# Performance work log

Hardware: AMD Instinct MI355X
Metric: run time of the kernel (lower is better)

## Reference

```python
import jax, jax.numpy as jnp
import numpy as np

D, L, H, DK, DV = 768, 512, 12, 64, 64
EPS = 1e-6

def setup_inputs() -> dict:
    key = jax.random.key(0)
    ks = jax.random.split(key, 14)
    def xn(k, shape):
        # xavier_normal: std = sqrt(2/(fan_in+fan_out))
        std = (2.0 / (shape[0] + shape[1])) ** 0.5
        return jax.random.normal(k, shape, dtype=jnp.float32) * std
    B = 8
    return {
        "Q": jax.random.normal(ks[0], (B, L, D), dtype=jnp.float32),
        "K": jax.random.normal(ks[1], (B, L, D), dtype=jnp.float32),
        "V": jax.random.normal(ks[2], (B, L, D), dtype=jnp.float32),
        "W_q": xn(ks[3], (D, H * DK)),
        "W_k": xn(ks[4], (D, H * DK)),
        "W_v": xn(ks[5], (D, H * DV)),
        "W_pos": xn(ks[6], (L, L)),
        "W_neg": xn(ks[7], (L, L)),
        "W_o": xn(ks[8], (H * DV, D)),
        "W_o2": xn(ks[9], (H * DV, D)),
        "w1": xn(ks[10], (D, D)),
        "b1": jnp.zeros((D,), dtype=jnp.float32),
        "w2": xn(ks[11], (D, D)),
        "b2": jnp.zeros((D,), dtype=jnp.float32),
    }

def reference(Q, K, V, W_q, W_k, W_v, W_pos, W_neg, W_o, W_o2, w1, b1, w2, b2):
    B, Lq, _ = Q.shape
    q = (Q @ W_q).reshape(B, Lq, H, DK)  # [B,L,H,dk]
    k = (K @ W_k).reshape(B, Lq, H, DK)
    v = (V @ W_v).reshape(B, Lq, H, DV)
    temp = DK ** 0.5 + EPS
    QK = jnp.einsum('bqhd,bkhd->bhqk', q, k) / temp  # [B,H,L,L]
    # einsum 'bqk,kk->bqk' == multiply by diagonal of W_pos/W_neg along key axis
    dpos = jnp.diagonal(W_pos)  # [L]
    dneg = jnp.diagonal(W_neg)
    sp = jax.nn.softmax(QK * dpos, axis=-1)
    sn = -jax.nn.softmax(-(QK * dneg), axis=-1)
    Vp = jnp.einsum('bhqk,bkhd->bqhd', sp, v).reshape(B, Lq, H * DV)
    Vn = jnp.einsum('bhqk,bkhd->bqhd', sn, v).reshape(B, Lq, H * DV)
    out_pos = Vp @ W_o
    out_neg = Vn @ W_o2
    def ffn(X):
        return jax.nn.relu(X @ w1 + b1) @ w2 + b2
    X_pos = Q + out_pos
    X_neg = Q + out_neg
    return (ffn(X_pos) + X_pos, ffn(X_neg) + X_neg)
```

## Files before the change

kernel.cpp:

```cpp
#include <hip/hip_runtime.h>
#include <hip/hip_bf16.h>
#include <math.h>

typedef __bf16 bf16_t;
typedef __bf16 bf16x4 __attribute__((ext_vector_type(4)));
typedef __bf16 bf16x8 __attribute__((ext_vector_type(8)));
typedef float f32x4 __attribute__((ext_vector_type(4)));

#define MFMA16(a, b, c) __builtin_amdgcn_mfma_f32_16x16x32_bf16((a), (b), (c), 0, 0, 0)
#define EXP2F(x) __builtin_amdgcn_exp2f(x)

__device__ __forceinline__ void gll16(const void* g, void* lds) {
    __builtin_amdgcn_global_load_lds((const __attribute__((address_space(1))) void*)g,
                                     (__attribute__((address_space(3))) void*)lds, 16, 0, 0);
}

struct PrepPtrs {
    const float* csrc[3];
    bf16_t* cdst[3];
    const float* wsrc[7];
    bf16_t* wdst[7];
};

__global__ __launch_bounds__(256) void prep_kernel(PrepPtrs p) {
    const int bx = blockIdx.x, tid = threadIdx.x;
    if (bx < 4608) {
        const int t = bx / 1536, i = (bx - t * 1536) * 256 + tid;
        const float4 u = ((const float4*)p.csrc[t])[i * 2];
        const float4 v = ((const float4*)p.csrc[t])[i * 2 + 1];
        bf16x8 o;
        o[0] = (bf16_t)u.x; o[1] = (bf16_t)u.y; o[2] = (bf16_t)u.z; o[3] = (bf16_t)u.w;
        o[4] = (bf16_t)v.x; o[5] = (bf16_t)v.y; o[6] = (bf16_t)v.z; o[7] = (bf16_t)v.w;
        ((bf16x8*)p.cdst[t])[i] = o;
    } else {
        __shared__ float t[32][33];
        const int q = bx - 4608, wz = q / 576, rem = q - wz * 576;
        const int bxx = rem % 24, byy = rem / 24;
        const float* src = p.wsrc[wz];
        bf16_t* dst = p.wdst[wz];
        const int tx = tid & 31, ty = tid >> 5;
        const int x = bxx * 32 + tx;
        const int y0 = byy * 32;
#pragma unroll
        for (int j = 0; j < 4; ++j)
            t[ty + j * 8][tx] = src[(size_t)(y0 + ty + j * 8) * 768 + x];
        __syncthreads();
        const int ox = byy * 32 + tx;
        const int oy0 = bxx * 32;
#pragma unroll
        for (int j = 0; j < 4; ++j)
            dst[(size_t)(oy0 + ty + j * 8) * 768 + ox] = (bf16_t)t[tx][ty + j * 8];
    }
}

struct GemmB {
    const bf16_t* A[3];
    const bf16_t* Bt[3];
    const float* bias;
    const float* Res[3];
    const bf16_t* ResB[3];
    float* Cf[3];
    bf16_t* Cb[3];
    bf16_t* VtOut;
};

template <bool HAS_BIAS, bool RELU, int RESMODE, int OUTMODE, bool VTZ = false>
__global__ __launch_bounds__(256, 3) void gemm2(GemmB p, int M, int K, int N) {
    __shared__ __align__(16) bf16_t As[128 * 64];
    __shared__ __align__(16) bf16_t Bs[96 * 64];
    const int z = blockIdx.z;
    const bf16_t* __restrict__ A = p.A[z];
    const bf16_t* __restrict__ Bt = p.Bt[z];
    const int tid = threadIdx.x, w = tid >> 6, l = tid & 63, l16 = l & 15, lk = l >> 4;
    const int wr = w >> 1, wc = w & 1;

    const int gx = gridDim.x, nwg = gx * gridDim.y;
    int flat = blockIdx.x + gx * blockIdx.y;
    flat = (flat & 7) * (nwg >> 3) + (flat >> 3);
    const int row0 = (flat / gx) * 128, col0 = (flat % gx) * 96;
    f32x4 acc[4][3] = {};

    const int lofs = l * 16;
    size_t aEl[4], bEl[3];
#pragma unroll
    for (int i = 0; i < 4; ++i) {
        const int off = (w * 4 + i) * 1024 + lofs;
        const int row = off >> 7;
        const int ch = ((off >> 4) & 7) ^ (row & 7);
        aEl[i] = (size_t)(row0 + row) * K + ch * 8;
    }
#pragma unroll
    for (int i = 0; i < 3; ++i) {
        const int off = (w * 3 + i) * 1024 + lofs;
        const int row = off >> 7;
        const int ch = ((off >> 4) & 7) ^ (row & 7);
        bEl[i] = (size_t)(col0 + row) * K + ch * 8;
    }

    for (int k0 = 0; k0 < K; k0 += 64) {
        __syncthreads();
#pragma unroll
        for (int i = 0; i < 4; ++i)
            gll16(A + aEl[i] + k0, (char*)As + (w * 4 + i) * 1024);
#pragma unroll
        for (int i = 0; i < 3; ++i)
            gll16(Bt + bEl[i] + k0, (char*)Bs + (w * 3 + i) * 1024);
        __syncthreads();

#pragma unroll
        for (int kk = 0; kk < 2; ++kk) {
            bf16x8 af[4], bfr[3];
#pragma unroll
            for (int mt = 0; mt < 4; ++mt) {
                const int ar = wr * 64 + mt * 16 + l16;
                af[mt] = *(const bf16x8*)((const char*)As + ar * 128 +
                                          (((kk * 4 + lk) ^ (ar & 7)) << 4));
            }
#pragma unroll
            for (int nt = 0; nt < 3; ++nt) {
                const int br = wc * 48 + nt * 16 + l16;
                bfr[nt] = *(const bf16x8*)((const char*)Bs + br * 128 +
                                           (((kk * 4 + lk) ^ (br & 7)) << 4));
            }
#pragma unroll
            for (int mt = 0; mt < 4; ++mt)
#pragma unroll
                for (int nt = 0; nt < 3; ++nt)
                    acc[mt][nt] = MFMA16(af[mt], bfr[nt], acc[mt][nt]);
        }
    }

    if constexpr (VTZ) {
        if (z == 2) {
            const int b = row0 >> 9;
            const int lb0 = (row0 & 511) + wr * 64;
#pragma unroll
            for (int mt = 0; mt < 4; ++mt)
#pragma unroll
                for (int nt = 0; nt < 3; ++nt) {
                    const int col = col0 + wc * 48 + nt * 16 + l16;
                    const int hh = col >> 6, dd = col & 63;
                    bf16x4 v;
#pragma unroll
                    for (int i = 0; i < 4; ++i) v[i] = (bf16_t)acc[mt][nt][i];
                    const size_t o =
                        (((size_t)(b * 12 + hh) * 64 + dd) << 9) + lb0 + mt * 16 + lk * 4;
                    *(bf16x4*)(p.VtOut + o) = v;
                }
            return;
        }
    }

#pragma unroll
    for (int mt = 0; mt < 4; ++mt)
#pragma unroll
        for (int nt = 0; nt < 3; ++nt)
#pragma unroll
            for (int i = 0; i < 4; ++i) {
                const int row = row0 + wr * 64 + mt * 16 + lk * 4 + i;
                const int col = col0 + wc * 48 + nt * 16 + l16;
                float val = acc[mt][nt][i];
                if constexpr (HAS_BIAS) val += p.bias[col];
                if constexpr (RELU) val = fmaxf(val, 0.0f);
                const size_t o = (size_t)row * N + col;
                if constexpr (RESMODE == 1) val += p.Res[z][o];
                if constexpr (RESMODE == 2) val += (float)p.ResB[z][o];
                if constexpr (OUTMODE == 0) p.Cf[z][o] = val;
                else p.Cb[z][o] = (bf16_t)val;
            }
}

__global__ __launch_bounds__(256, 3) void attn_kernel(const bf16_t* __restrict__ qb,
                                                      const bf16_t* __restrict__ kb,
                                                      const bf16_t* __restrict__ Vt,
                                                      const float* __restrict__ Wpos,
                                                      const float* __restrict__ Wneg,
                                                      bf16_t* __restrict__ Vpb,
                                                      bf16_t* __restrict__ Vnb) {
    __shared__ __align__(16) bf16_t Ks[2][64 * 64];
    __shared__ __align__(16) bf16_t Vs[2][64 * 64];
    __shared__ __align__(16) bf16_t Ps[4][16][72];
    const int tid = threadIdx.x, w = tid >> 6, l = tid & 63, l16 = l & 15, lk = l >> 4;
    const int rg = w >> 1, sgn = w & 1;
    const int bh = blockIdx.x, qt = blockIdx.y, b = bh / 12, h = bh % 12;
    const int q0 = qt * 32 + rg * 16;
    const float SC = 1.4426950408889634f / (8.0f + 1e-6f);
    const float sc = sgn ? -SC : SC;
    const float* __restrict__ Wd = sgn ? Wneg : Wpos;

    const size_t qbase = ((size_t)(b * 512 + q0)) * 768 + h * 64;
    const bf16x8 qf0 = *(const bf16x8*)(qb + qbase + (size_t)l16 * 768 + lk * 8);
    const bf16x8 qf1 = *(const bf16x8*)(qb + qbase + (size_t)l16 * 768 + 32 + lk * 8);

    const size_t kbase0 = ((size_t)b * 512) * 768 + h * 64;
    const size_t vtb = (size_t)bh * 64 * 512;
    size_t kEl[2], vEl[2];
    int seg[2];
#pragma unroll
    for (int i = 0; i < 2; ++i) {
        seg[i] = w * 2 + i;
        const int off = seg[i] * 1024 + l * 16;
        const int row = off >> 7, slot = (off >> 4) & 7;
        kEl[i] = (size_t)row * 768 + (size_t)((slot ^ (row & 7)) * 8);
        vEl[i] = (size_t)row * 512 + (size_t)((slot ^ (row & 7)) * 8);
    }

    auto stage = [&](int c, int buf) {
#pragma unroll
        for (int i = 0; i < 2; ++i) {
            gll16(kb + kbase0 + (size_t)c * 64 * 768 + kEl[i], (char*)&Ks[buf][0] + seg[i] * 1024);
            gll16(Vt + vtb + (size_t)c * 64 + vEl[i], (char*)&Vs[buf][0] + seg[i] * 1024);
        }
    };

    f32x4 pacc[4] = {};
    float sm[4] = {0, 0, 0, 0};

    stage(0, 0);
    __syncthreads();

    for (int c = 0; c < 8; ++c) {
        const int buf = c & 1;
        if (c < 7) stage(c + 1, buf ^ 1);

        float dv[4];
#pragma unroll
        for (int nt = 0; nt < 4; ++nt)
            dv[nt] = Wd[(size_t)(c * 64 + nt * 16 + l16) * 513] * sc;

        f32x4 sacc[4] = {};
        __builtin_amdgcn_s_setprio(1);
#pragma unroll
        for (int nt = 0; nt < 4; ++nt) {
            const int kr = nt * 16 + l16;
            const bf16x8 kv0 =
                *(const bf16x8*)((const char*)&Ks[buf][0] + kr * 128 + ((lk ^ (kr & 7)) << 4));
            const bf16x8 kv1 =
                *(const bf16x8*)((const char*)&Ks[buf][0] + kr * 128 + (((4 + lk) ^ (kr & 7)) << 4));
            sacc[nt] = MFMA16(qf0, kv0, sacc[nt]);
            sacc[nt] = MFMA16(qf1, kv1, sacc[nt]);
        }
        __builtin_amdgcn_s_setprio(0);

#pragma unroll
        for (int nt = 0; nt < 4; ++nt)
#pragma unroll
            for (int i = 0; i < 4; ++i) {
                const float e = EXP2F(sacc[nt][i] * dv[nt]);
                Ps[w][lk * 4 + i][nt * 16 + l16] = (bf16_t)e;
                sm[i] += e;
            }

        __builtin_amdgcn_s_setprio(1);
#pragma unroll
        for (int kt = 0; kt < 2; ++kt) {
            const bf16x8 pa = *(const bf16x8*)&Ps[w][l16][kt * 32 + lk * 8];
#pragma unroll
            for (int nd = 0; nd < 4; ++nd) {
                const int dr = nd * 16 + l16;
                const bf16x8 vv = *(const bf16x8*)((const char*)&Vs[buf][0] + dr * 128 +
                                                   (((kt * 4 + lk) ^ (dr & 7)) << 4));
                pacc[nd] = MFMA16(pa, vv, pacc[nd]);
            }
        }
        __builtin_amdgcn_s_setprio(0);

        if (c < 7) __syncthreads();
    }

#pragma unroll
    for (int off = 1; off < 16; off <<= 1)
#pragma unroll
        for (int i = 0; i < 4; ++i) sm[i] += __shfl_xor(sm[i], off, 64);

    bf16_t* __restrict__ Out = sgn ? Vnb : Vpb;
#pragma unroll
    for (int i = 0; i < 4; ++i) {
        const float r = (sgn ? -1.0f : 1.0f) / sm[i];
        const size_t o = ((size_t)(b * 512 + q0 + lk * 4 + i)) * 768 + h * 64;
#pragma unroll
        for (int nd = 0; nd < 4; ++nd) Out[o + nd * 16 + l16] = (bf16_t)(pacc[nd][i] * r);
    }
}

extern "C" void kernel_launch(void* const* d_in, const int* in_sizes, int n_in,
                              void* d_out, int out_size, void* d_ws, size_t ws_size,
                              hipStream_t stream) {
    const float* Q = (const float*)d_in[0];
    const float* K = (const float*)d_in[1];
    const float* V = (const float*)d_in[2];
    const float* W_q = (const float*)d_in[3];
    const float* W_k = (const float*)d_in[4];
    const float* W_v = (const float*)d_in[5];
    const float* Wpos = (const float*)d_in[6];
    const float* Wneg = (const float*)d_in[7];
    const float* W_o = (const float*)d_in[8];
    const float* W_o2 = (const float*)d_in[9];
    const float* w1 = (const float*)d_in[10];
    const float* b1 = (const float*)d_in[11];
    const float* w2 = (const float*)d_in[12];
    const float* b2 = (const float*)d_in[13];
    float* out = (float*)d_out;

    char* ws = (char*)d_ws;
    const size_t act_b = (size_t)4096 * 768 * 2;
    bf16_t* Qb = (bf16_t*)(ws + 0 * act_b);
    bf16_t* Kb = (bf16_t*)(ws + 1 * act_b);
    bf16_t* Vb = (bf16_t*)(ws + 2 * act_b);
    bf16_t* qb = (bf16_t*)(ws + 4 * act_b);
    bf16_t* kb = (bf16_t*)(ws + 5 * act_b);
    bf16_t* Vt = (bf16_t*)(ws + 6 * act_b);
    bf16_t* Wt[7];
    for (int i = 0; i < 7; ++i) Wt[i] = (bf16_t*)(ws + 7 * act_b + (size_t)i * 768 * 768 * 2);
    bf16_t* Vpb = Qb;
    bf16_t* Vnb = Kb;
    bf16_t* Xb = Vb;
    bf16_t* Hb = qb;

    PrepPtrs pp;
    pp.csrc[0] = Q; pp.csrc[1] = K; pp.csrc[2] = V;
    pp.cdst[0] = Qb; pp.cdst[1] = Kb; pp.cdst[2] = Vb;
    pp.wsrc[0] = W_q; pp.wsrc[1] = W_k; pp.wsrc[2] = W_v;
    pp.wsrc[3] = W_o; pp.wsrc[4] = W_o2; pp.wsrc[5] = w1; pp.wsrc[6] = w2;
    for (int i = 0; i < 7; ++i) pp.wdst[i] = Wt[i];
    prep_kernel<<<8640, 256, 0, stream>>>(pp);

    {
        GemmB g = {};
        g.A[0] = Qb; g.A[1] = Kb; g.A[2] = Vb;
        g.Bt[0] = Wt[0]; g.Bt[1] = Wt[1]; g.Bt[2] = Wt[2];
        g.Cb[0] = qb; g.Cb[1] = kb;
        g.VtOut = Vt;
        gemm2<false, false, 0, 1, true><<<dim3(8, 32, 3), 256, 0, stream>>>(g, 4096, 768, 768);
    }

    attn_kernel<<<dim3(96, 16), 256, 0, stream>>>(qb, kb, Vt, Wpos, Wneg, Vpb, Vnb);

    {
        GemmB g = {};
        g.A[0] = Vpb; g.A[1] = Vnb;
        g.Bt[0] = Wt[3]; g.Bt[1] = Wt[4];
        g.Res[0] = Q; g.Res[1] = Q;
        g.Cb[0] = Xb; g.Cb[1] = Xb + (size_t)4096 * 768;
        gemm2<false, false, 1, 1><<<dim3(8, 32, 2), 256, 0, stream>>>(g, 4096, 768, 768);
    }

    {
        GemmB g = {};
        g.A[0] = Xb;
        g.Bt[0] = Wt[5];
        g.bias = b1;
        g.Cb[0] = Hb;
        gemm2<true, true, 0, 1><<<dim3(8, 64, 1), 256, 0, stream>>>(g, 8192, 768, 768);
    }

    {
        GemmB g = {};
        g.A[0] = Hb;
        g.Bt[0] = Wt[6];
        g.bias = b2;
        g.ResB[0] = Xb;
        g.Cf[0] = out;
        gemm2<true, false, 2, 0><<<dim3(8, 64, 1), 256, 0, stream>>>(g, 8192, 768, 768);
    }
}
```

Baseline: 128.3 us.

## Double attention query tile per wave and precompute scaled diagonal vectors

```diff
diff --git a/kernel.cpp b/kernel.cpp
--- a/kernel.cpp
+++ b/kernel.cpp
@@ -20,6 +20,8 @@
     bf16_t* cdst[3];
     const float* wsrc[7];
     bf16_t* wdst[7];
+    const float* dsrc[2];
+    float* ddst[2];
 };
 
 __global__ __launch_bounds__(256) void prep_kernel(PrepPtrs p) {
@@ -32,7 +34,7 @@
         o[0] = (bf16_t)u.x; o[1] = (bf16_t)u.y; o[2] = (bf16_t)u.z; o[3] = (bf16_t)u.w;
         o[4] = (bf16_t)v.x; o[5] = (bf16_t)v.y; o[6] = (bf16_t)v.z; o[7] = (bf16_t)v.w;
         ((bf16x8*)p.cdst[t])[i] = o;
-    } else {
+    } else if (bx < 8640) {
         __shared__ float t[32][33];
         const int q = bx - 4608, wz = q / 576, rem = q - wz * 576;
         const int bxx = rem % 24, byy = rem / 24;
@@ -50,6 +52,13 @@
 #pragma unroll
         for (int j = 0; j < 4; ++j)
             dst[(size_t)(oy0 + ty + j * 8) * 768 + ox] = (bf16_t)t[tx][ty + j * 8];
+    } else {
+        const int s = bx - 8640;
+        const float SC = 1.4426950408889634f / (8.0f + 1e-6f);
+        const float sc = s ? -SC : SC;
+        const float* src = p.dsrc[s];
+        float* dst = p.ddst[s];
+        for (int i = tid; i < 512; i += 256) dst[i] = src[(size_t)i * 513] * sc;
     }
 }
 
@@ -173,24 +182,27 @@
 __global__ __launch_bounds__(256, 3) void attn_kernel(const bf16_t* __restrict__ qb,
                                                       const bf16_t* __restrict__ kb,
                                                       const bf16_t* __restrict__ Vt,
-                                                      const float* __restrict__ Wpos,
-                                                      const float* __restrict__ Wneg,
+                                                      const float* __restrict__ dPos,
+                                                      const float* __restrict__ dNeg,
                                                       bf16_t* __restrict__ Vpb,
                                                       bf16_t* __restrict__ Vnb) {
     __shared__ __align__(16) bf16_t Ks[2][64 * 64];
     __shared__ __align__(16) bf16_t Vs[2][64 * 64];
-    __shared__ __align__(16) bf16_t Ps[4][16][72];
+    __shared__ __align__(16) bf16_t Ps[4][32][72];
     const int tid = threadIdx.x, w = tid >> 6, l = tid & 63, l16 = l & 15, lk = l >> 4;
-    const int rg = w >> 1, sgn = w & 1;
+    const int rh = w >> 1, sgn = w & 1;
     const int bh = blockIdx.x, qt = blockIdx.y, b = bh / 12, h = bh % 12;
-    const int q0 = qt * 32 + rg * 16;
-    const float SC = 1.4426950408889634f / (8.0f + 1e-6f);
-    const float sc = sgn ? -SC : SC;
-    const float* __restrict__ Wd = sgn ? Wneg : Wpos;
+    const int q0 = qt * 64 + rh * 32;
+    const float* __restrict__ Wd = sgn ? dNeg : dPos;
 
     const size_t qbase = ((size_t)(b * 512 + q0)) * 768 + h * 64;
-    const bf16x8 qf0 = *(const bf16x8*)(qb + qbase + (size_t)l16 * 768 + lk * 8);
-    const bf16x8 qf1 = *(const bf16x8*)(qb + qbase + (size_t)l16 * 768 + 32 + lk * 8);
+    bf16x8 qf[2][2];
+#pragma unroll
+    for (int rt = 0; rt < 2; ++rt)
+#pragma unroll
+        for (int ks = 0; ks < 2; ++ks)
+            qf[rt][ks] =
+                *(const bf16x8*)(qb + qbase + (size_t)(rt * 16 + l16) * 768 + ks * 32 + lk * 8);
 
     const size_t kbase0 = ((size_t)b * 512) * 768 + h * 64;
     const size_t vtb = (size_t)bh * 64 * 512;
@@ -213,8 +225,8 @@
         }
     };
 
-    f32x4 pacc[4] = {};
-    float sm[4] = {0, 0, 0, 0};
+    f32x4 pacc[2][4] = {};
+    float sm[2][4] = {};
 
     stage(0, 0);
     __syncthreads();
@@ -225,10 +237,9 @@
 
         float dv[4];
 #pragma unroll
-        for (int nt = 0; nt < 4; ++nt)
-            dv[nt] = Wd[(size_t)(c * 64 + nt * 16 + l16) * 513] * sc;
-
-        f32x4 sacc[4] = {};
+        for (int nt = 0; nt < 4; ++nt) dv[nt] = Wd[c * 64 + nt * 16 + l16];
+
+        f32x4 sacc[2][4] = {};
         __builtin_amdgcn_s_setprio(1);
 #pragma unroll
         for (int nt = 0; nt < 4; ++nt) {
@@ -237,30 +248,36 @@
                 *(const bf16x8*)((const char*)&Ks[buf][0] + kr * 128 + ((lk ^ (kr & 7)) << 4));
             const bf16x8 kv1 =
                 *(const bf16x8*)((const char*)&Ks[buf][0] + kr * 128 + (((4 + lk) ^ (kr & 7)) << 4));
-            sacc[nt] = MFMA16(qf0, kv0, sacc[nt]);
-            sacc[nt] = MFMA16(qf1, kv1, sacc[nt]);
+            sacc[0][nt] = MFMA16(qf[0][0], kv0, sacc[0][nt]);
+            sacc[0][nt] = MFMA16(qf[0][1], kv1, sacc[0][nt]);
+            sacc[1][nt] = MFMA16(qf[1][0], kv0, sacc[1][nt]);
+            sacc[1][nt] = MFMA16(qf[1][1], kv1, sacc[1][nt]);
         }
         __builtin_amdgcn_s_setprio(0);
 
 #pragma unroll
-        for (int nt = 0; nt < 4; ++nt)
-#pragma unroll
-            for (int i = 0; i < 4; ++i) {
-                const float e = EXP2F(sacc[nt][i] * dv[nt]);
-                Ps[w][lk * 4 + i][nt * 16 + l16] = (bf16_t)e;
-                sm[i] += e;
-            }
+        for (int rt = 0; rt < 2; ++rt)
+#pragma unroll
+            for (int nt = 0; nt < 4; ++nt)
+#pragma unroll
+                for (int i = 0; i < 4; ++i) {
+                    const float e = EXP2F(sacc[rt][nt][i] * dv[nt]);
+                    Ps[w][rt * 16 + lk * 4 + i][nt * 16 + l16] = (bf16_t)e;
+                    sm[rt][i] += e;
+                }
 
         __builtin_amdgcn_s_setprio(1);
 #pragma unroll
         for (int kt = 0; kt < 2; ++kt) {
-            const bf16x8 pa = *(const bf16x8*)&Ps[w][l16][kt * 32 + lk * 8];
+            const bf16x8 pa0 = *(const bf16x8*)&Ps[w][l16][kt * 32 + lk * 8];
+            const bf16x8 pa1 = *(const bf16x8*)&Ps[w][16 + l16][kt * 32 + lk * 8];
 #pragma unroll
             for (int nd = 0; nd < 4; ++nd) {
                 const int dr = nd * 16 + l16;
                 const bf16x8 vv = *(const bf16x8*)((const char*)&Vs[buf][0] + dr * 128 +
                                                    (((kt * 4 + lk) ^ (dr & 7)) << 4));
-                pacc[nd] = MFMA16(pa, vv, pacc[nd]);
+                pacc[0][nd] = MFMA16(pa0, vv, pacc[0][nd]);
+                pacc[1][nd] = MFMA16(pa1, vv, pacc[1][nd]);
             }
         }
         __builtin_amdgcn_s_setprio(0);
@@ -271,16 +288,20 @@
 #pragma unroll
     for (int off = 1; off < 16; off <<= 1)
 #pragma unroll
-        for (int i = 0; i < 4; ++i) sm[i] += __shfl_xor(sm[i], off, 64);
+        for (int rt = 0; rt < 2; ++rt)
+#pragma unroll
+            for (int i = 0; i < 4; ++i) sm[rt][i] += __shfl_xor(sm[rt][i], off, 64);
 
     bf16_t* __restrict__ Out = sgn ? Vnb : Vpb;
 #pragma unroll
-    for (int i = 0; i < 4; ++i) {
-        const float r = (sgn ? -1.0f : 1.0f) / sm[i];
-        const size_t o = ((size_t)(b * 512 + q0 + lk * 4 + i)) * 768 + h * 64;
-#pragma unroll
-        for (int nd = 0; nd < 4; ++nd) Out[o + nd * 16 + l16] = (bf16_t)(pacc[nd][i] * r);
-    }
+    for (int rt = 0; rt < 2; ++rt)
+#pragma unroll
+        for (int i = 0; i < 4; ++i) {
+            const float r = (sgn ? -1.0f : 1.0f) / sm[rt][i];
+            const size_t o = ((size_t)(b * 512 + q0 + rt * 16 + lk * 4 + i)) * 768 + h * 64;
+#pragma unroll
+            for (int nd = 0; nd < 4; ++nd) Out[o + nd * 16 + l16] = (bf16_t)(pacc[rt][nd][i] * r);
+        }
 }
 
 extern "C" void kernel_launch(void* const* d_in, const int* in_sizes, int n_in,
@@ -304,6 +325,7 @@
 
     char* ws = (char*)d_ws;
     const size_t act_b = (size_t)4096 * 768 * 2;
+    const size_t wt_b = (size_t)768 * 768 * 2;
     bf16_t* Qb = (bf16_t*)(ws + 0 * act_b);
     bf16_t* Kb = (bf16_t*)(ws + 1 * act_b);
     bf16_t* Vb = (bf16_t*)(ws + 2 * act_b);
@@ -311,7 +333,9 @@
     bf16_t* kb = (bf16_t*)(ws + 5 * act_b);
     bf16_t* Vt = (bf16_t*)(ws + 6 * act_b);
     bf16_t* Wt[7];
-    for (int i = 0; i < 7; ++i) Wt[i] = (bf16_t*)(ws + 7 * act_b + (size_t)i * 768 * 768 * 2);
+    for (int i = 0; i < 7; ++i) Wt[i] = (bf16_t*)(ws + 7 * act_b + (size_t)i * wt_b);
+    float* dPos = (float*)(ws + 7 * act_b + 7 * wt_b);
+    float* dNeg = dPos + 512;
     bf16_t* Vpb = Qb;
     bf16_t* Vnb = Kb;
     bf16_t* Xb = Vb;
@@ -323,7 +347,9 @@
     pp.wsrc[0] = W_q; pp.wsrc[1] = W_k; pp.wsrc[2] = W_v;
     pp.wsrc[3] = W_o; pp.wsrc[4] = W_o2; pp.wsrc[5] = w1; pp.wsrc[6] = w2;
     for (int i = 0; i < 7; ++i) pp.wdst[i] = Wt[i];
-    prep_kernel<<<8640, 256, 0, stream>>>(pp);
+    pp.dsrc[0] = Wpos; pp.dsrc[1] = Wneg;
+    pp.ddst[0] = dPos; pp.ddst[1] = dNeg;
+    prep_kernel<<<8642, 256, 0, stream>>>(pp);
 
     {
         GemmB g = {};
@@ -334,7 +360,7 @@
         gemm2<false, false, 0, 1, true><<<dim3(8, 32, 3), 256, 0, stream>>>(g, 4096, 768, 768);
     }
 
-    attn_kernel<<<dim3(96, 16), 256, 0, stream>>>(qb, kb, Vt, Wpos, Wneg, Vpb, Vnb);
+    attn_kernel<<<dim3(96, 8), 256, 0, stream>>>(qb, kb, Vt, dPos, dNeg, Vpb, Vnb);
 
     {
         GemmB g = {};
```

Measured after the change: 120.0 us. 6.4% less time.
